# Kernel tuning notes

Hardware: AMD Instinct MI355X
Metric: run time of the kernel (lower is better)

The kernel has to match this reference:

```python
import jax, jax.numpy as jnp
import numpy as np

GAMMA = 0.002


def setup_inputs() -> dict:
    key = jax.random.key(0)
    k1, k2, k3, k4 = jax.random.split(key, 4)
    n, m, d = 16384, 8192, 512
    X = jax.random.normal(k1, (n, d), dtype=jnp.float32)
    Y = jax.random.normal(k2, (m, d), dtype=jnp.float32)
    # nn.Linear(m, 1): weight (1, m), bias (1,), default torch init ~ U(-1/sqrt(m), 1/sqrt(m))
    bound = 1.0 / np.sqrt(m)
    W = jax.random.uniform(k3, (1, m), dtype=jnp.float32, minval=-bound, maxval=bound)
    b = jax.random.uniform(k4, (1,), dtype=jnp.float32, minval=-bound, maxval=bound)
    return {"X": X, "Y": Y, "W": W, "b": b}


def reference(X, Y, W, b):
    # RBF Gram matrix via the GEMM squared-distance trick:
    x2 = jnp.sum(X * X, axis=-1, keepdims=True)          # (n, 1)
    y2 = jnp.sum(Y * Y, axis=-1)[None, :]                # (1, m)
    xy = jnp.einsum('nd,md->nm', X, Y)                   # (n, m)
    sq = jnp.maximum(x2 + y2 - 2.0 * xy, 0.0)            # clamp tiny negatives
    K = jnp.exp(-GAMMA * sq)                             # (n, m)
    # Linear(m -> 1) then squeeze(-1)
    out = jnp.einsum('nm,om->no', K, W) + b              # (n, 1)
    return out[:, 0]
```

## Files before the change

kernel.cpp:

```cpp
#include <hip/hip_runtime.h>
#include <hip/hip_bf16.h>


#define GAMMA 0.002f

typedef __bf16 bf16x8 __attribute__((ext_vector_type(8)));
typedef float  f32x4  __attribute__((ext_vector_type(4)));
typedef __attribute__((address_space(3))) void lds_void_t;
typedef __attribute__((address_space(1))) const void gl_void_t;

__global__ __launch_bounds__(256) void prep_x(const float* __restrict__ src,
                                              __bf16* __restrict__ dst,
                                              float* __restrict__ fac) {
    const int wid  = threadIdx.x >> 6;
    const int lane = threadIdx.x & 63;
    const int row  = blockIdx.x * 4 + wid;
    const float4* s = reinterpret_cast<const float4*>(src + (size_t)row * 512);
    float4 v0 = s[lane * 2];
    float4 v1 = s[lane * 2 + 1];
    float acc = v0.x * v0.x + v0.y * v0.y + v0.z * v0.z + v0.w * v0.w
              + v1.x * v1.x + v1.y * v1.y + v1.z * v1.z + v1.w * v1.w;
    bf16x8 o;
    o[0] = (__bf16)v0.x; o[1] = (__bf16)v0.y; o[2] = (__bf16)v0.z; o[3] = (__bf16)v0.w;
    o[4] = (__bf16)v1.x; o[5] = (__bf16)v1.y; o[6] = (__bf16)v1.z; o[7] = (__bf16)v1.w;
    *reinterpret_cast<bf16x8*>(dst + (size_t)row * 512 + lane * 8) = o;
#pragma unroll
    for (int off = 32; off >= 1; off >>= 1) acc += __shfl_xor(acc, off, 64);
    if (lane == 0) fac[row] = __expf(-GAMMA * acc);
}

__global__ __launch_bounds__(256) void prep_y(const float* __restrict__ src,
                                              __bf16* __restrict__ dst,
                                              float* __restrict__ fac,
                                              const float* __restrict__ W) {
    const int wid  = threadIdx.x >> 6;
    const int lane = threadIdx.x & 63;
    const int m    = blockIdx.x * 4 + wid;
    const float4* s = reinterpret_cast<const float4*>(src + (size_t)m * 512);
    float4 v0 = s[lane * 2];
    float4 v1 = s[lane * 2 + 1];
    float acc = v0.x * v0.x + v0.y * v0.y + v0.z * v0.z + v0.w * v0.w
              + v1.x * v1.x + v1.y * v1.y + v1.z * v1.z + v1.w * v1.w;
    bf16x8 o;
    o[0] = (__bf16)v0.x; o[1] = (__bf16)v0.y; o[2] = (__bf16)v0.z; o[3] = (__bf16)v0.w;
    o[4] = (__bf16)v1.x; o[5] = (__bf16)v1.y; o[6] = (__bf16)v1.z; o[7] = (__bf16)v1.w;
    const size_t idx = ((size_t)(lane >> 2) * 512 + (m >> 4)) * 512
                     + ((lane & 3) * 16 + (m & 15)) * 8;
    *reinterpret_cast<bf16x8*>(dst + idx) = o;
#pragma unroll
    for (int off = 32; off >= 1; off >>= 1) acc += __shfl_xor(acc, off, 64);
    if (lane == 0) fac[m] = __expf(-GAMMA * acc) * W[m];
}

__global__ void init_out(float* __restrict__ out, const float* __restrict__ b, int n) {
    int i = blockIdx.x * blockDim.x + threadIdx.x;
    if (i < n) out[i] = b[0];
}


#define LOADB(B, C) do { \
    const int q_ = (C) & 15, p_ = (C) >> 4; \
    const __bf16* bp_ = Ybt + ((size_t)q_ * 512 + cbgBase + p_ * 16) * 512 + lane8; \
    B[0] = *reinterpret_cast<const bf16x8*>(bp_); \
    B[1] = *reinterpret_cast<const bf16x8*>(bp_ + 512); \
} while (0)

#define READA(A, Q) do { \
    _Pragma("unroll") \
    for (int rb = 0; rb < 4; ++rb) \
        A[rb] = *reinterpret_cast<const bf16x8*>( \
            &smem[(Q) * 4096 + rb * 1024 + lane16]); \
} while (0)

#define MFMA8(A, B) do { \
    __builtin_amdgcn_s_setprio(1); \
    _Pragma("unroll") \
    for (int rb = 0; rb < 4; ++rb) \
        _Pragma("unroll") \
        for (int cb = 0; cb < 2; ++cb) \
            acc[rb][cb] = __builtin_amdgcn_mfma_f32_16x16x32_bf16( \
                A[rb], B[cb], acc[rb][cb], 0, 0, 0); \
    __builtin_amdgcn_s_setprio(0); \
} while (0)

__global__ __launch_bounds__(512, 4) void rbf_gemm(
    const __bf16* __restrict__ Xb, const __bf16* __restrict__ Ybt,
    const float* __restrict__ ex, const float* __restrict__ cwp,
    float* __restrict__ out) {
    __shared__ __align__(128) char smem[81920];

    const int tid  = threadIdx.x;
    const int wid  = tid >> 6;
    const int lane = tid & 63;

    const int pid = blockIdx.x;
    const int xcd = pid & 7;
    const int j   = pid >> 3;
    const int ch  = xcd & 1;
    const int rg  = (xcd >> 1) * 64 + j;
    const int rowBase = rg * 64;
    const int colBase = ch * 4096;
    const int cbgBase = ch * 256 + wid * 2;

    const int l15 = lane & 15, l4 = lane >> 4;
    const int lane16 = lane * 16;
    const int lane8  = lane * 8;

#pragma unroll
    for (int i = 0; i < 8; ++i) {
        const int blk = wid * 8 + i;
        const int q = blk >> 2, rb = blk & 3;
        const __bf16* src = Xb + (size_t)(rowBase + rb * 16 + l15) * 512 + q * 32 + l4 * 8;
        __builtin_amdgcn_global_load_lds((gl_void_t*)src,
            (lds_void_t*)(smem + q * 4096 + rb * 1024), 16, 0, 0);
    }
#pragma unroll
    for (int i = 0; i < 2; ++i)
        __builtin_amdgcn_global_load_lds(
            (gl_void_t*)(cwp + colBase + wid * 512 + i * 256 + lane * 4),
            (lds_void_t*)(smem + 65536 + wid * 2048 + i * 1024), 16, 0, 0);
    asm volatile("s_waitcnt vmcnt(0)");
    __builtin_amdgcn_s_barrier();

    f32x4 acc[4][2] = {};
    float rowsum[4][4] = {};

    bf16x8 A0[4], A1[4], B0[2], B1[2];
    LOADB(B0, 0);

    for (int cc = 0; cc < 128; ++cc) {
        const int ce = 2 * cc, co = 2 * cc + 1;
        LOADB(B1, co);
        READA(A0, ce & 15);
        MFMA8(A0, B0);
        LOADB(B0, (co + 1) & 255);
        READA(A1, co & 15);
        MFMA8(A1, B1);
        if ((cc & 7) == 7) {
            const int p = cc >> 3;
            float cv[2];
#pragma unroll
            for (int cb = 0; cb < 2; ++cb)
                cv[cb] = *reinterpret_cast<const float*>(
                    &smem[65536 + (p * 256 + wid * 32 + cb * 16 + l15) * 4]);
#pragma unroll
            for (int rb = 0; rb < 4; ++rb)
#pragma unroll
                for (int i2 = 0; i2 < 4; ++i2) {
                    rowsum[rb][i2] += __expf(0.004f * acc[rb][0][i2]) * cv[0]
                                    + __expf(0.004f * acc[rb][1][i2]) * cv[1];
                }
#pragma unroll
            for (int rb = 0; rb < 4; ++rb) {
                acc[rb][0] = (f32x4){0.f, 0.f, 0.f, 0.f};
                acc[rb][1] = (f32x4){0.f, 0.f, 0.f, 0.f};
            }
        }
    }

#pragma unroll
    for (int rb = 0; rb < 4; ++rb)
#pragma unroll
        for (int i2 = 0; i2 < 4; ++i2) {
            float s = rowsum[rb][i2];
#pragma unroll
            for (int off = 1; off < 16; off <<= 1) s += __shfl_xor(s, off, 64);
            if (l15 == 0) {
                const int n = rowBase + rb * 16 + l4 * 4 + i2;
                atomicAdd(&out[n], ex[n] * s);
            }
        }
}

extern "C" void kernel_launch(void* const* d_in, const int* in_sizes, int n_in,
                              void* d_out, int out_size, void* d_ws, size_t ws_size,
                              hipStream_t stream) {
    const float* X = (const float*)d_in[0];
    const float* Y = (const float*)d_in[1];
    const float* W = (const float*)d_in[2];
    const float* b = (const float*)d_in[3];
    float* out = (float*)d_out;

    char* ws = (char*)d_ws;
    __bf16* Xb  = (__bf16*)(ws);
    __bf16* Ybt = (__bf16*)(ws + 16777216);
    float*  ex  = (float*)(ws + 16777216 + 8388608);
    float*  cw  = (float*)(ws + 16777216 + 8388608 + 65536);

    prep_x<<<4096, 256, 0, stream>>>(X, Xb, ex);
    prep_y<<<2048, 256, 0, stream>>>(Y, Ybt, cw, W);
    init_out<<<64, 256, 0, stream>>>(out, b, 16384);
    rbf_gemm<<<512, 512, 0, stream>>>(Xb, Ybt, ex, cw, out);
}
```

Baseline: 154.1 us.

## Switch RBF GEMM to 32x32x16 MFMA with matching Y and LDS layouts

Replaces the 16x16x32 bf16 MFMA tiling (8 instructions per k-step on 4x2 16x16 tiles) with 32x32x16 MFMAs on two 32x32 output tiles per wave. The Y transpose layout written by prep_y, the B fragment loads, the LDS staging of X, the epilogue exp/weight accumulation and the final cross-lane reduction are all rewritten to match the new fragment layout. The aim is fewer MFMA issues and better operand reuse per instruction. The cost is larger accumulator registers and a more complex row-index mapping, which could hurt occupancy or correctness.

```diff
diff --git a/kernel.cpp b/kernel.cpp
--- a/kernel.cpp
+++ b/kernel.cpp
@@ -5,7 +5,7 @@
 #define GAMMA 0.002f
 
 typedef __bf16 bf16x8 __attribute__((ext_vector_type(8)));
-typedef float  f32x4  __attribute__((ext_vector_type(4)));
+typedef float  f32x16 __attribute__((ext_vector_type(16)));
 typedef __attribute__((address_space(3))) void lds_void_t;
 typedef __attribute__((address_space(1))) const void gl_void_t;
 
@@ -44,8 +44,8 @@
     bf16x8 o;
     o[0] = (__bf16)v0.x; o[1] = (__bf16)v0.y; o[2] = (__bf16)v0.z; o[3] = (__bf16)v0.w;
     o[4] = (__bf16)v1.x; o[5] = (__bf16)v1.y; o[6] = (__bf16)v1.z; o[7] = (__bf16)v1.w;
-    const size_t idx = ((size_t)(lane >> 2) * 512 + (m >> 4)) * 512
-                     + ((lane & 3) * 16 + (m & 15)) * 8;
+    const size_t idx = ((size_t)(m >> 5) * 32 + (lane >> 1)) * 512
+                     + ((lane & 1) * 32 + (m & 31)) * 8;
     *reinterpret_cast<bf16x8*>(dst + idx) = o;
 #pragma unroll
     for (int off = 32; off >= 1; off >>= 1) acc += __shfl_xor(acc, off, 64);
@@ -60,26 +60,24 @@
 
 #define LOADB(B, C) do { \
     const int q_ = (C) & 15, p_ = (C) >> 4; \
-    const __bf16* bp_ = Ybt + ((size_t)q_ * 512 + cbgBase + p_ * 16) * 512 + lane8; \
+    const __bf16* bp_ = Ybt + ((size_t)(cbg32 + p_ * 8) * 32 + 2 * q_) * 512 + lane8; \
     B[0] = *reinterpret_cast<const bf16x8*>(bp_); \
     B[1] = *reinterpret_cast<const bf16x8*>(bp_ + 512); \
 } while (0)
 
-#define READA(A, Q) do { \
+#define READA(AF, Q) do { \
     _Pragma("unroll") \
-    for (int rb = 0; rb < 4; ++rb) \
-        A[rb] = *reinterpret_cast<const bf16x8*>( \
-            &smem[(Q) * 4096 + rb * 1024 + lane16]); \
+    for (int j = 0; j < 4; ++j) \
+        AF[j] = *reinterpret_cast<const bf16x8*>( \
+            &smem[(Q) * 4096 + j * 1024 + lane16]); \
 } while (0)
 
-#define MFMA8(A, B) do { \
+#define MFMA4(AF, B) do { \
     __builtin_amdgcn_s_setprio(1); \
-    _Pragma("unroll") \
-    for (int rb = 0; rb < 4; ++rb) \
-        _Pragma("unroll") \
-        for (int cb = 0; cb < 2; ++cb) \
-            acc[rb][cb] = __builtin_amdgcn_mfma_f32_16x16x32_bf16( \
-                A[rb], B[cb], acc[rb][cb], 0, 0, 0); \
+    acc[0] = __builtin_amdgcn_mfma_f32_32x32x16_bf16(AF[0], B[0], acc[0], 0, 0, 0); \
+    acc[1] = __builtin_amdgcn_mfma_f32_32x32x16_bf16(AF[1], B[0], acc[1], 0, 0, 0); \
+    acc[0] = __builtin_amdgcn_mfma_f32_32x32x16_bf16(AF[2], B[1], acc[0], 0, 0, 0); \
+    acc[1] = __builtin_amdgcn_mfma_f32_32x32x16_bf16(AF[3], B[1], acc[1], 0, 0, 0); \
     __builtin_amdgcn_s_setprio(0); \
 } while (0)
 
@@ -99,74 +97,67 @@
     const int ch  = xcd & 1;
     const int rg  = (xcd >> 1) * 64 + j;
     const int rowBase = rg * 64;
-    const int colBase = ch * 4096;
-    const int cbgBase = ch * 256 + wid * 2;
+    const int cbg32   = ch * 128 + wid;
 
-    const int l15 = lane & 15, l4 = lane >> 4;
+    const int l31 = lane & 31, lhi = lane >> 5;
     const int lane16 = lane * 16;
     const int lane8  = lane * 8;
 
 #pragma unroll
     for (int i = 0; i < 8; ++i) {
         const int blk = wid * 8 + i;
-        const int q = blk >> 2, rb = blk & 3;
-        const __bf16* src = Xb + (size_t)(rowBase + rb * 16 + l15) * 512 + q * 32 + l4 * 8;
+        const int q = blk >> 2, sub = blk & 3;
+        const int ksp = sub >> 1, rt = sub & 1;
+        const __bf16* src = Xb + (size_t)(rowBase + rt * 32 + l31) * 512
+                          + q * 32 + ksp * 16 + lhi * 8;
         __builtin_amdgcn_global_load_lds((gl_void_t*)src,
-            (lds_void_t*)(smem + q * 4096 + rb * 1024), 16, 0, 0);
+            (lds_void_t*)(smem + blk * 1024), 16, 0, 0);
     }
 #pragma unroll
     for (int i = 0; i < 2; ++i)
         __builtin_amdgcn_global_load_lds(
-            (gl_void_t*)(cwp + colBase + wid * 512 + i * 256 + lane * 4),
+            (gl_void_t*)(cwp + ch * 4096 + wid * 512 + i * 256 + lane * 4),
             (lds_void_t*)(smem + 65536 + wid * 2048 + i * 1024), 16, 0, 0);
     asm volatile("s_waitcnt vmcnt(0)");
     __builtin_amdgcn_s_barrier();
 
-    f32x4 acc[4][2] = {};
-    float rowsum[4][4] = {};
+    f32x16 acc[2] = {};
+    float rowsum[2][16] = {};
 
-    bf16x8 A0[4], A1[4], B0[2], B1[2];
+    bf16x8 AF[4], B0[2], B1[2];
     LOADB(B0, 0);
 
     for (int cc = 0; cc < 128; ++cc) {
         const int ce = 2 * cc, co = 2 * cc + 1;
         LOADB(B1, co);
-        READA(A0, ce & 15);
-        MFMA8(A0, B0);
+        READA(AF, ce & 15);
+        MFMA4(AF, B0);
         LOADB(B0, (co + 1) & 255);
-        READA(A1, co & 15);
-        MFMA8(A1, B1);
+        READA(AF, co & 15);
+        MFMA4(AF, B1);
         if ((cc & 7) == 7) {
             const int p = cc >> 3;
-            float cv[2];
+            const float cv = *reinterpret_cast<const float*>(
+                &smem[65536 + ((p * 8 + wid) * 32 + l31) * 4]);
 #pragma unroll
-            for (int cb = 0; cb < 2; ++cb)
-                cv[cb] = *reinterpret_cast<const float*>(
-                    &smem[65536 + (p * 256 + wid * 32 + cb * 16 + l15) * 4]);
+            for (int rt = 0; rt < 2; ++rt)
 #pragma unroll
-            for (int rb = 0; rb < 4; ++rb)
-#pragma unroll
-                for (int i2 = 0; i2 < 4; ++i2) {
-                    rowsum[rb][i2] += __expf(0.004f * acc[rb][0][i2]) * cv[0]
-                                    + __expf(0.004f * acc[rb][1][i2]) * cv[1];
-                }
-#pragma unroll
-            for (int rb = 0; rb < 4; ++rb) {
-                acc[rb][0] = (f32x4){0.f, 0.f, 0.f, 0.f};
-                acc[rb][1] = (f32x4){0.f, 0.f, 0.f, 0.f};
-            }
+                for (int r = 0; r < 16; ++r)
+                    rowsum[rt][r] += __expf(0.004f * acc[rt][r]) * cv;
+            acc[0] = f32x16{};
+            acc[1] = f32x16{};
         }
     }
 
 #pragma unroll
-    for (int rb = 0; rb < 4; ++rb)
+    for (int rt = 0; rt < 2; ++rt)
 #pragma unroll
-        for (int i2 = 0; i2 < 4; ++i2) {
-            float s = rowsum[rb][i2];
+        for (int r = 0; r < 16; ++r) {
+            float s = rowsum[rt][r];
 #pragma unroll
-            for (int off = 1; off < 16; off <<= 1) s += __shfl_xor(s, off, 64);
-            if (l15 == 0) {
-                const int n = rowBase + rb * 16 + l4 * 4 + i2;
+            for (int off = 1; off < 32; off <<= 1) s += __shfl_xor(s, off, 64);
+            if (l31 == 0) {
+                const int n = rowBase + rt * 32 + (r & 3) + 8 * (r >> 2) + 4 * lhi;
                 atomicAdd(&out[n], ex[n] * s);
             }
         }
```

After: 183.0 us. 1.19x slower.
